# Performance work log

Measured on AMD Instinct MI355X. Metric: run time of the kernel, lower is better.

Reference implementation:

```python
import jax, jax.numpy as jnp
import numpy as np

DIM = 384
KEY_DIM = 32
NUM_HEADS = 8
ATTN_RATIO = 4
RESOLUTION = 48
N_TOKENS = RESOLUTION * RESOLUTION  # 2304
D_V = ATTN_RATIO * KEY_DIM          # 128
NH_KD = NUM_HEADS * KEY_DIM         # 256
DH = NUM_HEADS * D_V                # 1024
SCALE = KEY_DIM ** (-0.5)


def _make_bias_idxs(res):
    # offset (|dy|,|dx|) -> unique id via dy*res+dx (bijection onto 0..res^2-1)
    coords = np.stack(np.meshgrid(np.arange(res), np.arange(res), indexing='ij'), -1).reshape(-1, 2)
    off = np.abs(coords[:, None, :] - coords[None, :, :])  # (N,N,2)
    return (off[..., 0] * res + off[..., 1]).astype(np.int32)  # (N,N)


def setup_inputs() -> dict:
    key = jax.random.key(0)
    ks = jax.random.split(key, 12)
    f32 = jnp.float32
    x = jax.random.normal(ks[0], (N_TOKENS, DIM, 1, 1), dtype=f32)
    # 1x1 convs == linear layers: weight (out, in), bias (out,)
    q_w = jax.random.normal(ks[1], (NH_KD, DIM), dtype=f32) * 0.05
    q_b = jax.random.normal(ks[2], (NH_KD,), dtype=f32) * 0.02
    k_w = jax.random.normal(ks[3], (NH_KD, DIM), dtype=f32) * 0.05
    k_b = jax.random.normal(ks[4], (NH_KD,), dtype=f32) * 0.02
    v_w = jax.random.normal(ks[5], (DH, DIM), dtype=f32) * 0.05
    v_b = jax.random.normal(ks[6], (DH,), dtype=f32) * 0.02
    proj_w = jax.random.normal(ks[7], (DIM, DH), dtype=f32) * 0.05
    proj_b = jax.random.normal(ks[8], (DIM,), dtype=f32) * 0.02
    attention_biases = jax.random.normal(ks[9], (NUM_HEADS, 1, RESOLUTION * RESOLUTION), dtype=f32) * 0.02
    bias_idxs = jnp.asarray(_make_bias_idxs(RESOLUTION))  # (N,N) int32
    return {
        'x': x, 'q_w': q_w, 'q_b': q_b, 'k_w': k_w, 'k_b': k_b,
        'v_w': v_w, 'v_b': v_b, 'proj_w': proj_w, 'proj_b': proj_b,
        'attention_biases': attention_biases, 'bias_idxs': bias_idxs,
    }


def reference(x, q_w, q_b, k_w, k_b, v_w, v_b, proj_w, proj_b, attention_biases, bias_idxs):
    N = x.shape[0]
    xf = x.reshape(N, DIM)  # H=W=1 so 1x1 conv is a matmul
    q = (xf @ q_w.T + q_b).reshape(N, NUM_HEADS, KEY_DIM).transpose(1, 0, 2)  # (H,N,kd)
    k = (xf @ k_w.T + k_b).reshape(N, NUM_HEADS, KEY_DIM).transpose(1, 0, 2)  # (H,N,kd)
    v = (xf @ v_w.T + v_b).reshape(N, NUM_HEADS, D_V).transpose(1, 0, 2)      # (H,N,dv)
    bias = attention_biases[:, 0, :][:, bias_idxs]  # gather -> (H,N,N)
    attn = jnp.einsum('hnd,hmd->hnm', q, k) * SCALE + bias
    attn = jax.nn.softmax(attn, axis=-1)
    out = jnp.einsum('hnm,hmd->hnd', attn, v)       # (H,N,dv)
    out = out.transpose(1, 0, 2).reshape(N, DH)
    y = out @ proj_w.T + proj_b
    return y.reshape(N, DIM, 1, 1)
```

## Files before the change

kernel.cpp:

```cpp
#include <hip/hip_runtime.h>

typedef unsigned short u16;
typedef unsigned int u32;
typedef short bf16x8 __attribute__((ext_vector_type(8)));
typedef float f32x4 __attribute__((ext_vector_type(4)));

#define SCALE 0.17677669529663687f

static __device__ __forceinline__ float bf2f(u16 h) {
    u32 u = ((u32)h) << 16;
    float f;
    __builtin_memcpy(&f, &u, 4);
    return f;
}
static __device__ __forceinline__ u16 f2bf(float f) {
    u32 u;
    __builtin_memcpy(&u, &f, 4);
    u += 0x7fffu + ((u >> 16) & 1u);
    return (u16)(u >> 16);
}
static __device__ __forceinline__ float IN1(const void* p, int idx, int md) {
    return md ? ((const float*)p)[idx] : bf2f(((const u16*)p)[idx]);
}

__global__ void detect_kernel(const unsigned int* __restrict__ x, int* __restrict__ mode)
{
    int lane = threadIdx.x;
    int cnt = 0;
    for (int i = lane; i < 4096; i += 64) {
        unsigned int e = (x[i] >> 7) & 0xFFu;
        cnt += (e >= 100u && e <= 140u) ? 1 : 0;
    }
    for (int off = 32; off; off >>= 1) cnt += __shfl_down(cnt, off);
    if (lane == 0) *mode = (cnt < 2048) ? 1 : 0;
}

struct ConvArgs {
    const void* src[9];
    int ofs[10];
};
__global__ __launch_bounds__(256) void convert_all(
    ConvArgs a, u16* __restrict__ dst, const int* __restrict__ mode, int total)
{
    const int md = *mode;
    int base = (blockIdx.x * 256 + threadIdx.x) * 8;
    for (int e = 0; e < 8; e++) {
        int i = base + e;
        if (i >= total) return;
        int t = 0;
        for (int j = 1; j < 9; j++) t += (i >= a.ofs[j]) ? 1 : 0;
        int idx = i - a.ofs[t];
        dst[i] = md ? f2bf(((const float*)a.src[t])[idx])
                    : ((const u16*)a.src[t])[idx];
    }
}

__global__ __launch_bounds__(256) void qkv_kernel(
    const u16* __restrict__ x,
    const u16* __restrict__ qw, const u16* __restrict__ qb,
    const u16* __restrict__ kw, const u16* __restrict__ kb,
    const u16* __restrict__ vw, const u16* __restrict__ vb,
    u16* __restrict__ qo, u16* __restrict__ ko, u16* __restrict__ vo)
{
    __shared__ __align__(16) short As[64 * 40];
    __shared__ __align__(16) short Bs[128 * 40];
    const int tid  = threadIdx.x;
    const int lane = tid & 63;
    const int w    = tid >> 6;
    const int l15  = lane & 15, quad = lane >> 4;
    const int mT = blockIdx.y, nT = blockIdx.x;

    const u16* wp; const u16* bp; u16* op; int r0, ldo;
    if (nT < 2)      { wp = qw; bp = qb; op = qo; r0 = nT * 128;       ldo = 256;  }
    else if (nT < 4) { wp = kw; bp = kb; op = ko; r0 = (nT - 2) * 128; ldo = 256;  }
    else             { wp = vw; bp = vb; op = vo; r0 = (nT - 4) * 128; ldo = 1024; }

    const int wm = (w >> 1) * 32, wn = (w & 1) * 64;
    const f32x4 vz = {0.f, 0.f, 0.f, 0.f};
    f32x4 acc[2][4];
    for (int mi = 0; mi < 2; mi++)
        for (int ni = 0; ni < 4; ni++) acc[mi][ni] = vz;

    const int arow = tid >> 2, seg = tid & 3;
    for (int kk = 0; kk < 384; kk += 32) {
        *(bf16x8*)&As[arow * 40 + seg * 8] =
            *(const bf16x8*)&x[(mT * 64 + arow) * 384 + kk + seg * 8];
        for (int i = 0; i < 2; i++) {
            int row = i * 64 + arow;
            *(bf16x8*)&Bs[row * 40 + seg * 8] =
                *(const bf16x8*)&wp[(r0 + row) * 384 + kk + seg * 8];
        }
        __syncthreads();
        bf16x8 af[2], bfr[4];
        for (int mi = 0; mi < 2; mi++)
            af[mi] = *(const bf16x8*)&As[(wm + mi * 16 + l15) * 40 + quad * 8];
        for (int ni = 0; ni < 4; ni++)
            bfr[ni] = *(const bf16x8*)&Bs[(wn + ni * 16 + l15) * 40 + quad * 8];
        for (int mi = 0; mi < 2; mi++)
            for (int ni = 0; ni < 4; ni++)
                acc[mi][ni] = __builtin_amdgcn_mfma_f32_16x16x32_bf16(
                    af[mi], bfr[ni], acc[mi][ni], 0, 0, 0);
        __syncthreads();
    }

    for (int ni = 0; ni < 4; ni++) {
        int col = r0 + wn + ni * 16 + l15;
        float bias = bf2f(bp[col]);
        for (int mi = 0; mi < 2; mi++) {
            int rowb = mT * 64 + wm + mi * 16 + quad * 4;
            for (int rr = 0; rr < 4; rr++)
                op[(rowb + rr) * ldo + col] = f2bf(acc[mi][ni][rr] + bias);
        }
    }
}

__global__ __launch_bounds__(256) void ktile_kernel(
    const u16* __restrict__ k, u16* __restrict__ kT)
{
    int c = blockIdx.x * 256 + threadIdx.x;
    int lane = c & 63;
    int kt2  = (c >> 6) % 144;
    int head = (c >> 6) / 144;
    int l15 = lane & 15, quad = lane >> 4;
    *(bf16x8*)&kT[c * 8] =
        *(const bf16x8*)&k[(kt2 * 16 + l15) * 256 + head * 32 + quad * 8];
}

__global__ __launch_bounds__(256) void vtile_kernel(
    const u16* __restrict__ v, u16* __restrict__ vTt)
{
    int c = blockIdx.x * 256 + threadIdx.x;
    int lane = c & 63;
    int vb   = (c >> 6) & 7;
    int kt   = (c >> 9) % 72;
    int head = (c >> 9) / 72;
    int l15 = lane & 15, quad = lane >> 4;
    bf16x8 val;
    for (int j = 0; j < 8; j++)
        val[j] = (short)v[(kt * 32 + quad * 8 + j) * 1024 + head * 128 + vb * 16 + l15];
    *(bf16x8*)&vTt[c * 8] = val;
}

__global__ __launch_bounds__(256) void attn_v6(
    const u16* __restrict__ qbuf, const u16* __restrict__ kT,
    const u16* __restrict__ vTt,  const void* __restrict__ ab,
    u16* __restrict__ obuf, const int* __restrict__ mode)
{
    __shared__ __align__(16) float abl[2304];
    __shared__ __align__(16) u16   Pl[4][2][640];
    __shared__ __align__(16) float osh[2048];
    __shared__ __align__(16) float lsh[16];

    const int tid  = threadIdx.x;
    const int lane = tid & 63;
    const int w    = tid >> 6;
    const int l15  = lane & 15, quad = lane >> 4;
    const int head = blockIdx.y;
    const int q0   = blockIdx.x * 16;
    const int md   = *mode;

    for (int i = tid; i < 2304; i += 256) abl[i] = IN1(ab, head * 2304 + i, md);
    for (int i = tid; i < 2048; i += 256) osh[i] = 0.f;
    if (tid < 16) lsh[tid] = 0.f;
    __syncthreads();

    bf16x8 qfrag = *(const bf16x8*)&qbuf[(q0 + l15) * 256 + head * 32 + quad * 8];

    int qr[4], qc[4];
    for (int r = 0; r < 4; r++) {
        int qrow = q0 + quad * 4 + r;
        qr[r] = qrow / 48; qc[r] = qrow % 48;
    }

    const f32x4 vz = {0.f, 0.f, 0.f, 0.f};
    f32x4 o[8];
    for (int vb = 0; vb < 8; vb++) o[vb] = vz;
    float ls[4] = {0.f, 0.f, 0.f, 0.f};

    const int kstart = w * 576;
    const u16* kTb = kT  + head * 73728;
    const u16* vTb = vTt + head * 294912;
    const int t16 = kstart >> 4;
    const int vt0 = kstart >> 5;

    auto score_step = [&](int tt, bf16x8 a0, bf16x8 a1) {
        int kb = kstart + tt * 32;
        f32x4 s0 = __builtin_amdgcn_mfma_f32_16x16x32_bf16(qfrag, a0, vz, 0, 0, 0);
        f32x4 s1 = __builtin_amdgcn_mfma_f32_16x16x32_bf16(qfrag, a1, vz, 0, 0, 0);
        int k0 = kb + l15, k1 = k0 + 16;
        int kr0 = k0 / 48, kc0 = k0 % 48;
        int kr1 = k1 / 48, kc1 = k1 % 48;
        u16* P = &Pl[w][tt & 1][0];
        for (int r = 0; r < 4; r++) {
            float a0f = s0[r] * SCALE + abl[abs(qr[r] - kr0) * 48 + abs(qc[r] - kc0)];
            a0f = fminf(fmaxf(a0f, -60.f), 60.f);
            float p0 = __expf(a0f);
            ls[r] += p0;
            P[(quad * 4 + r) * 40 + l15] = f2bf(p0);
            float a1f = s1[r] * SCALE + abl[abs(qr[r] - kr1) * 48 + abs(qc[r] - kc1)];
            a1f = fminf(fmaxf(a1f, -60.f), 60.f);
            float p1 = __expf(a1f);
            ls[r] += p1;
            P[(quad * 4 + r) * 40 + 16 + l15] = f2bf(p1);
        }
    };

    {
        bf16x8 c0 = *(const bf16x8*)&kTb[((t16 + 0) * 64 + lane) * 8];
        bf16x8 c1 = *(const bf16x8*)&kTb[((t16 + 1) * 64 + lane) * 8];
        score_step(0, c0, c1);
    }
    bf16x8 kA0 = *(const bf16x8*)&kTb[((t16 + 2) * 64 + lane) * 8];
    bf16x8 kA1 = *(const bf16x8*)&kTb[((t16 + 3) * 64 + lane) * 8];

    for (int t = 0; t < 18; t++) {
        bf16x8 pf = *(const bf16x8*)&Pl[w][t & 1][l15 * 40 + quad * 8];

        bf16x8 vf[8];
        for (int vb = 0; vb < 8; vb++)
            vf[vb] = *(const bf16x8*)&vTb[(((vt0 + t) * 8 + vb) * 64 + lane) * 8];

        if (t < 17) {
            int nt = (t + 2 <= 17) ? (t + 2) : 17;
            bf16x8 kB0 = *(const bf16x8*)&kTb[((t16 + nt * 2) * 64 + lane) * 8];
            bf16x8 kB1 = *(const bf16x8*)&kTb[((t16 + nt * 2 + 1) * 64 + lane) * 8];
            score_step(t + 1, kA0, kA1);
            kA0 = kB0; kA1 = kB1;
        }

        for (int vb = 0; vb < 8; vb++)
            o[vb] = __builtin_amdgcn_mfma_f32_16x16x32_bf16(pf, vf[vb], o[vb], 0, 0, 0);
    }

    for (int r = 0; r < 4; r++)
        for (int off = 1; off < 16; off <<= 1)
            ls[r] += __shfl_xor(ls[r], off);

    for (int ph = 0; ph < 4; ph++) {
        if (w == ph) {
            for (int vb = 0; vb < 8; vb++)
                for (int r = 0; r < 4; r++)
                    osh[(quad * 4 + r) * 128 + vb * 16 + l15] += o[vb][r];
            if (l15 == 0)
                for (int r = 0; r < 4; r++) lsh[quad * 4 + r] += ls[r];
        }
        __syncthreads();
    }

    for (int i = tid; i < 2048; i += 256) {
        int row = i >> 7, dv = i & 127;
        obuf[(q0 + row) * 1024 + head * 128 + dv] = f2bf(osh[i] / lsh[row]);
    }
}

__global__ __launch_bounds__(256) void proj_kernel(
    const u16* __restrict__ ob, const u16* __restrict__ pw,
    const u16* __restrict__ pb, void* __restrict__ y, const int* __restrict__ mode)
{
    __shared__ __align__(16) short As[64 * 40];
    __shared__ __align__(16) short Bs[64 * 40];
    const int tid  = threadIdx.x;
    const int lane = tid & 63;
    const int w    = tid >> 6;
    const int l15  = lane & 15, quad = lane >> 4;
    const int mT = blockIdx.y, nT = blockIdx.x;
    const int wm = (w >> 1) * 32, wn = (w & 1) * 32;
    const int md = *mode;

    const f32x4 vz = {0.f, 0.f, 0.f, 0.f};
    f32x4 acc[2][2];
    for (int mi = 0; mi < 2; mi++)
        for (int ni = 0; ni < 2; ni++) acc[mi][ni] = vz;

    for (int kk = 0; kk < 1024; kk += 32) {
        int row = tid >> 2, seg = tid & 3;
        *(bf16x8*)&As[row * 40 + seg * 8] =
            *(const bf16x8*)&ob[(mT * 64 + row) * 1024 + kk + seg * 8];
        *(bf16x8*)&Bs[row * 40 + seg * 8] =
            *(const bf16x8*)&pw[(nT * 64 + row) * 1024 + kk + seg * 8];
        __syncthreads();
        bf16x8 af[2], bfr[2];
        for (int mi = 0; mi < 2; mi++)
            af[mi] = *(const bf16x8*)&As[(wm + mi * 16 + l15) * 40 + quad * 8];
        for (int ni = 0; ni < 2; ni++)
            bfr[ni] = *(const bf16x8*)&Bs[(wn + ni * 16 + l15) * 40 + quad * 8];
        for (int mi = 0; mi < 2; mi++)
            for (int ni = 0; ni < 2; ni++)
                acc[mi][ni] = __builtin_amdgcn_mfma_f32_16x16x32_bf16(
                    af[mi], bfr[ni], acc[mi][ni], 0, 0, 0);
        __syncthreads();
    }

    for (int ni = 0; ni < 2; ni++) {
        int col = nT * 64 + wn + ni * 16 + l15;
        float bias = bf2f(pb[col]);
        for (int mi = 0; mi < 2; mi++) {
            int rowb = mT * 64 + wm + mi * 16 + quad * 4;
            for (int rr = 0; rr < 4; rr++) {
                float val = acc[mi][ni][rr] + bias;
                int idx = (rowb + rr) * 384 + col;
                if (md) ((float*)y)[idx] = val;
                else    ((u16*)y)[idx]   = f2bf(val);
            }
        }
    }
}

extern "C" void kernel_launch(void* const* d_in, const int* in_sizes, int n_in,
                              void* d_out, int out_size, void* d_ws, size_t ws_size,
                              hipStream_t stream)
{
    const void *x = 0, *qw = 0, *qb = 0, *kw = 0, *kb = 0;
    const void *vw = 0, *vb = 0, *pw = 0, *pb = 0, *ab = 0;
    void* scratch = 0;

    for (int i = 0; i < n_in; i++) {
        const void* p = d_in[i];
        switch (in_sizes[i]) {
            case 884736:  x  = p; break;
            case 98304:   if (!qw) qw = p; else kw = p; break;
            case 256:     if (!qb) qb = p; else kb = p; break;
            case 393216:  if (!vw) vw = p; else pw = p; break;
            case 1024:    vb = p; break;
            case 384:     pb = p; break;
            case 18432:   ab = p; break;
            case 5308416: scratch = (void*)p; break;
        }
    }
    if (!scratch) scratch = d_ws;

    u16* arena = (u16*)scratch;
    u16* cx  = arena;
    u16* cqw = arena + 884736;
    u16* cqb = arena + 983040;
    u16* ckw = arena + 983296;
    u16* ckb = arena + 1081600;
    u16* cvw = arena + 1081856;
    u16* cvb = arena + 1475072;
    u16* cpw = arena + 1476096;
    u16* cpb = arena + 1869312;
    u16* q_bf = arena + 1869696;
    u16* k_bf = arena + 2459520;
    u16* v_bf = arena + 3049344;
    u16* vTt  = arena + 5408640;
    u16* ob   = arena + 7767936;
    u16* kT   = arena;
    int* mode = ((int*)scratch) + 5308400;

    detect_kernel<<<1, 64, 0, stream>>>((const unsigned int*)x, mode);

    ConvArgs ca;
    ca.src[0] = x;  ca.src[1] = qw; ca.src[2] = qb; ca.src[3] = kw; ca.src[4] = kb;
    ca.src[5] = vw; ca.src[6] = vb; ca.src[7] = pw; ca.src[8] = pb;
    ca.ofs[0] = 0;       ca.ofs[1] = 884736;  ca.ofs[2] = 983040;
    ca.ofs[3] = 983296;  ca.ofs[4] = 1081600; ca.ofs[5] = 1081856;
    ca.ofs[6] = 1475072; ca.ofs[7] = 1476096; ca.ofs[8] = 1869312;
    ca.ofs[9] = 1869696;
    convert_all<<<(1869696 / 8 + 255) / 256, 256, 0, stream>>>(ca, arena, mode, 1869696);

    qkv_kernel<<<dim3(12, 36), 256, 0, stream>>>(cx, cqw, cqb, ckw, ckb, cvw, cvb,
                                                 q_bf, k_bf, v_bf);
    ktile_kernel<<<288, 256, 0, stream>>>(k_bf, kT);
    vtile_kernel<<<1152, 256, 0, stream>>>(v_bf, vTt);
    attn_v6<<<dim3(144, 8), 256, 0, stream>>>(q_bf, kT, vTt, ab, ob, mode);
    proj_kernel<<<dim3(6, 36), 256, 0, stream>>>(ob, cpw, cpb, d_out, mode);
}
```

Baseline: 181.9 us.

## Fuse K/V retiling into QKV GEMM epilogue and widen GEMM K-steps

The QKV projection kernel now writes K and V straight into the tiled layouts the attention kernel consumes. This removes the separate ktile and vtile kernels, along with their extra global round trip and two launches. The QKV and projection GEMMs also stage larger K chunks (64 and 128) per shared-memory load, which cuts the number of barriers. The tiled epilogue stores are scattered 2-byte writes, and the larger LDS footprint may lower occupancy.

Measured after the change: 170.5 us. 6.3% less time.

```diff
diff --git a/kernel.cpp b/kernel.cpp
--- a/kernel.cpp
+++ b/kernel.cpp
@@ -60,20 +60,20 @@
     const u16* __restrict__ qw, const u16* __restrict__ qb,
     const u16* __restrict__ kw, const u16* __restrict__ kb,
     const u16* __restrict__ vw, const u16* __restrict__ vb,
-    u16* __restrict__ qo, u16* __restrict__ ko, u16* __restrict__ vo)
-{
-    __shared__ __align__(16) short As[64 * 40];
-    __shared__ __align__(16) short Bs[128 * 40];
+    u16* __restrict__ qo, u16* __restrict__ kT, u16* __restrict__ vTt)
+{
+    __shared__ __align__(16) short As[64 * 72];
+    __shared__ __align__(16) short Bs[128 * 72];
     const int tid  = threadIdx.x;
     const int lane = tid & 63;
     const int w    = tid >> 6;
     const int l15  = lane & 15, quad = lane >> 4;
     const int mT = blockIdx.y, nT = blockIdx.x;
 
-    const u16* wp; const u16* bp; u16* op; int r0, ldo;
-    if (nT < 2)      { wp = qw; bp = qb; op = qo; r0 = nT * 128;       ldo = 256;  }
-    else if (nT < 4) { wp = kw; bp = kb; op = ko; r0 = (nT - 2) * 128; ldo = 256;  }
-    else             { wp = vw; bp = vb; op = vo; r0 = (nT - 4) * 128; ldo = 1024; }
+    const u16* wp; const u16* bp; int r0, which;
+    if (nT < 2)      { wp = qw; bp = qb; r0 = nT * 128;       which = 0; }
+    else if (nT < 4) { wp = kw; bp = kb; r0 = (nT - 2) * 128; which = 1; }
+    else             { wp = vw; bp = vb; r0 = (nT - 4) * 128; which = 2; }
 
     const int wm = (w >> 1) * 32, wn = (w & 1) * 64;
     const f32x4 vz = {0.f, 0.f, 0.f, 0.f};
@@ -81,25 +81,28 @@
     for (int mi = 0; mi < 2; mi++)
         for (int ni = 0; ni < 4; ni++) acc[mi][ni] = vz;
 
-    const int arow = tid >> 2, seg = tid & 3;
-    for (int kk = 0; kk < 384; kk += 32) {
-        *(bf16x8*)&As[arow * 40 + seg * 8] =
-            *(const bf16x8*)&x[(mT * 64 + arow) * 384 + kk + seg * 8];
-        for (int i = 0; i < 2; i++) {
-            int row = i * 64 + arow;
-            *(bf16x8*)&Bs[row * 40 + seg * 8] =
-                *(const bf16x8*)&wp[(r0 + row) * 384 + kk + seg * 8];
-        }
-        __syncthreads();
-        bf16x8 af[2], bfr[4];
-        for (int mi = 0; mi < 2; mi++)
-            af[mi] = *(const bf16x8*)&As[(wm + mi * 16 + l15) * 40 + quad * 8];
-        for (int ni = 0; ni < 4; ni++)
-            bfr[ni] = *(const bf16x8*)&Bs[(wn + ni * 16 + l15) * 40 + quad * 8];
-        for (int mi = 0; mi < 2; mi++)
+    const int arow = tid >> 2, aseg = tid & 3;
+    const int brow = tid >> 1, bseg = tid & 1;
+
+    for (int kk = 0; kk < 384; kk += 64) {
+        for (int c = 0; c < 2; c++)
+            *(bf16x8*)&As[arow * 72 + aseg * 16 + c * 8] =
+                *(const bf16x8*)&x[(mT * 64 + arow) * 384 + kk + aseg * 16 + c * 8];
+        for (int c = 0; c < 4; c++)
+            *(bf16x8*)&Bs[brow * 72 + bseg * 32 + c * 8] =
+                *(const bf16x8*)&wp[(r0 + brow) * 384 + kk + bseg * 32 + c * 8];
+        __syncthreads();
+        for (int s = 0; s < 2; s++) {
+            bf16x8 af[2], bfr[4];
+            for (int mi = 0; mi < 2; mi++)
+                af[mi] = *(const bf16x8*)&As[(wm + mi * 16 + l15) * 72 + s * 32 + quad * 8];
             for (int ni = 0; ni < 4; ni++)
-                acc[mi][ni] = __builtin_amdgcn_mfma_f32_16x16x32_bf16(
-                    af[mi], bfr[ni], acc[mi][ni], 0, 0, 0);
+                bfr[ni] = *(const bf16x8*)&Bs[(wn + ni * 16 + l15) * 72 + s * 32 + quad * 8];
+            for (int mi = 0; mi < 2; mi++)
+                for (int ni = 0; ni < 4; ni++)
+                    acc[mi][ni] = __builtin_amdgcn_mfma_f32_16x16x32_bf16(
+                        af[mi], bfr[ni], acc[mi][ni], 0, 0, 0);
+        }
         __syncthreads();
     }
 
@@ -108,37 +111,23 @@
         float bias = bf2f(bp[col]);
         for (int mi = 0; mi < 2; mi++) {
             int rowb = mT * 64 + wm + mi * 16 + quad * 4;
-            for (int rr = 0; rr < 4; rr++)
-                op[(rowb + rr) * ldo + col] = f2bf(acc[mi][ni][rr] + bias);
-        }
-    }
-}
-
-__global__ __launch_bounds__(256) void ktile_kernel(
-    const u16* __restrict__ k, u16* __restrict__ kT)
-{
-    int c = blockIdx.x * 256 + threadIdx.x;
-    int lane = c & 63;
-    int kt2  = (c >> 6) % 144;
-    int head = (c >> 6) / 144;
-    int l15 = lane & 15, quad = lane >> 4;
-    *(bf16x8*)&kT[c * 8] =
-        *(const bf16x8*)&k[(kt2 * 16 + l15) * 256 + head * 32 + quad * 8];
-}
-
-__global__ __launch_bounds__(256) void vtile_kernel(
-    const u16* __restrict__ v, u16* __restrict__ vTt)
-{
-    int c = blockIdx.x * 256 + threadIdx.x;
-    int lane = c & 63;
-    int vb   = (c >> 6) & 7;
-    int kt   = (c >> 9) % 72;
-    int head = (c >> 9) / 72;
-    int l15 = lane & 15, quad = lane >> 4;
-    bf16x8 val;
-    for (int j = 0; j < 8; j++)
-        val[j] = (short)v[(kt * 32 + quad * 8 + j) * 1024 + head * 128 + vb * 16 + l15];
-    *(bf16x8*)&vTt[c * 8] = val;
+            for (int rr = 0; rr < 4; rr++) {
+                int tok = rowb + rr;
+                u16 val = f2bf(acc[mi][ni][rr] + bias);
+                if (which == 0) {
+                    qo[tok * 256 + col] = val;
+                } else if (which == 1) {
+                    int addr = (((col >> 5) * 144 + (tok >> 4)) << 9)
+                             + (((col & 31) >> 3) << 7) + ((tok & 15) << 3) + (col & 7);
+                    kT[addr] = val;
+                } else {
+                    int addr = ((((col >> 7) * 72 + (tok >> 5)) * 8 + ((col >> 4) & 7)) << 9)
+                             + (((tok >> 3) & 3) << 7) + ((col & 15) << 3) + (tok & 7);
+                    vTt[addr] = val;
+                }
+            }
+        }
+    }
 }
 
 __global__ __launch_bounds__(256) void attn_v6(
@@ -257,8 +246,8 @@
     const u16* __restrict__ ob, const u16* __restrict__ pw,
     const u16* __restrict__ pb, void* __restrict__ y, const int* __restrict__ mode)
 {
-    __shared__ __align__(16) short As[64 * 40];
-    __shared__ __align__(16) short Bs[64 * 40];
+    __shared__ __align__(16) short As[64 * 136];
+    __shared__ __align__(16) short Bs[64 * 136];
     const int tid  = threadIdx.x;
     const int lane = tid & 63;
     const int w    = tid >> 6;
@@ -272,22 +261,26 @@
     for (int mi = 0; mi < 2; mi++)
         for (int ni = 0; ni < 2; ni++) acc[mi][ni] = vz;
 
-    for (int kk = 0; kk < 1024; kk += 32) {
-        int row = tid >> 2, seg = tid & 3;
-        *(bf16x8*)&As[row * 40 + seg * 8] =
-            *(const bf16x8*)&ob[(mT * 64 + row) * 1024 + kk + seg * 8];
-        *(bf16x8*)&Bs[row * 40 + seg * 8] =
-            *(const bf16x8*)&pw[(nT * 64 + row) * 1024 + kk + seg * 8];
-        __syncthreads();
-        bf16x8 af[2], bfr[2];
-        for (int mi = 0; mi < 2; mi++)
-            af[mi] = *(const bf16x8*)&As[(wm + mi * 16 + l15) * 40 + quad * 8];
-        for (int ni = 0; ni < 2; ni++)
-            bfr[ni] = *(const bf16x8*)&Bs[(wn + ni * 16 + l15) * 40 + quad * 8];
-        for (int mi = 0; mi < 2; mi++)
+    const int row = tid >> 2, seg = tid & 3;
+    for (int kk = 0; kk < 1024; kk += 128) {
+        for (int c = 0; c < 4; c++) {
+            *(bf16x8*)&As[row * 136 + seg * 32 + c * 8] =
+                *(const bf16x8*)&ob[(mT * 64 + row) * 1024 + kk + seg * 32 + c * 8];
+            *(bf16x8*)&Bs[row * 136 + seg * 32 + c * 8] =
+                *(const bf16x8*)&pw[(nT * 64 + row) * 1024 + kk + seg * 32 + c * 8];
+        }
+        __syncthreads();
+        for (int s = 0; s < 4; s++) {
+            bf16x8 af[2], bfr[2];
+            for (int mi = 0; mi < 2; mi++)
+                af[mi] = *(const bf16x8*)&As[(wm + mi * 16 + l15) * 136 + s * 32 + quad * 8];
             for (int ni = 0; ni < 2; ni++)
-                acc[mi][ni] = __builtin_amdgcn_mfma_f32_16x16x32_bf16(
-                    af[mi], bfr[ni], acc[mi][ni], 0, 0, 0);
+                bfr[ni] = *(const bf16x8*)&Bs[(wn + ni * 16 + l15) * 136 + s * 32 + quad * 8];
+            for (int mi = 0; mi < 2; mi++)
+                for (int ni = 0; ni < 2; ni++)
+                    acc[mi][ni] = __builtin_amdgcn_mfma_f32_16x16x32_bf16(
+                        af[mi], bfr[ni], acc[mi][ni], 0, 0, 0);
+        }
         __syncthreads();
     }
 
@@ -340,11 +333,9 @@
     u16* cpw = arena + 1476096;
     u16* cpb = arena + 1869312;
     u16* q_bf = arena + 1869696;
-    u16* k_bf = arena + 2459520;
-    u16* v_bf = arena + 3049344;
-    u16* vTt  = arena + 5408640;
+    u16* kT   = arena + 2459520;
+    u16* vTt  = arena + 3049344;
     u16* ob   = arena + 7767936;
-    u16* kT   = arena;
     int* mode = ((int*)scratch) + 5308400;
 
     detect_kernel<<<1, 64, 0, stream>>>((const unsigned int*)x, mode);
@@ -359,9 +350,7 @@
     convert_all<<<(1869696 / 8 + 255) / 256, 256, 0, stream>>>(ca, arena, mode, 1869696);
 
     qkv_kernel<<<dim3(12, 36), 256, 0, stream>>>(cx, cqw, cqb, ckw, ckb, cvw, cvb,
-                                                 q_bf, k_bf, v_bf);
-    ktile_kernel<<<288, 256, 0, stream>>>(k_bf, kT);
-    vtile_kernel<<<1152, 256, 0, stream>>>(v_bf, vTt);
+                                                 q_bf, kT, vTt);
     attn_v6<<<dim3(144, 8), 256, 0, stream>>>(q_bf, kT, vTt, ab, ob, mode);
     proj_kernel<<<dim3(6, 36), 256, 0, stream>>>(ob, cpw, cpb, d_out, mode);
 }
```
